# Performance work log

Hardware: AMD Instinct MI355X
Metric: run time of the kernel (lower is better)

Reference implementation:

```python
import jax, jax.numpy as jnp
import numpy as np

B, C, H, W = 4, 128, 128, 128
K = 9          # 3x3 kernel taps
TAU, BETA = 0.5, 10.0


def conv3x3(x, w, b):
    # x: (B,Cin,H,W), w: (Cout,Cin,3,3), stride 1, padding 1
    y = jax.lax.conv_general_dilated(
        x, w, window_strides=(1, 1), padding=((1, 1), (1, 1)),
        dimension_numbers=('NCHW', 'OIHW', 'NCHW'))
    return y + b[None, :, None, None]


def bilinear_sample(x, py, px):
    # x: (B,C,H,W); py,px: (B,K,H,W) fractional coords -> (B,C,K,H,W), zero outside
    Hi, Wi = x.shape[2], x.shape[3]
    y0 = jnp.floor(py); x0 = jnp.floor(px)
    y1 = y0 + 1.0;      x1 = x0 + 1.0
    ly = py - y0; lx = px - x0
    hy = 1.0 - ly; hx = 1.0 - lx
    xf = x.reshape(x.shape[0], x.shape[1], -1)  # (B,C,HW)

    def corner(yc, xc, wgt):
        valid = (yc >= 0) & (yc <= Hi - 1) & (xc >= 0) & (xc <= Wi - 1)
        yi = jnp.clip(yc, 0, Hi - 1).astype(jnp.int32)
        xi = jnp.clip(xc, 0, Wi - 1).astype(jnp.int32)
        idx = (yi * Wi + xi).reshape(yc.shape[0], -1)  # (B, K*H*W)
        g = jax.vmap(lambda f, i: f[:, i])(xf, idx)    # (B,C,K*H*W)
        g = g.reshape(x.shape[0], x.shape[1], *yc.shape[1:])  # (B,C,K,H,W)
        return g * (wgt * valid.astype(wgt.dtype))[:, None]

    return (corner(y0, x0, hy * hx) + corner(y0, x1, hy * lx)
            + corner(y1, x0, ly * hx) + corner(y1, x1, ly * lx))


def modulated_dcn(x, offset, mask, w, b):
    # offset: (B,2K,H,W) layout (dy,dx) per tap; mask: (B,K,H,W)
    Bn, Cn, Hn, Wn = x.shape
    off = offset.reshape(Bn, K, 2, Hn, Wn)
    dy, dx = off[:, :, 0], off[:, :, 1]
    ky, kx = jnp.meshgrid(jnp.arange(3), jnp.arange(3), indexing='ij')
    base_y = (ky.reshape(-1) - 1).astype(x.dtype)  # dilation=1, padding=1, stride=1
    base_x = (kx.reshape(-1) - 1).astype(x.dtype)
    hh = jnp.arange(Hn, dtype=x.dtype)
    ww = jnp.arange(Wn, dtype=x.dtype)
    py = hh[None, None, :, None] + base_y[None, :, None, None] + dy  # (B,K,H,W)
    px = ww[None, None, None, :] + base_x[None, :, None, None] + dx
    samp = bilinear_sample(x, py, px) * mask[:, None]  # (B,C,K,H,W)
    out = jnp.einsum('bckhw,ock->bohw', samp, w.reshape(w.shape[0], w.shape[1], K))
    return out + b[None, :, None, None]


def setup_inputs() -> dict:
    key = jax.random.key(0)
    ks = jax.random.split(key, 8)
    x = jax.random.normal(ks[0], (B, C, H, W), dtype=jnp.float32)
    U = jax.random.uniform(ks[1], (B, 1, H, W), dtype=jnp.float32)
    # conv_offset_mask: (3*K, C+1, 3, 3); small scale -> offsets of O(1) pixel
    w_om = jax.random.normal(ks[2], (3 * K, C + 1, 3, 3), dtype=jnp.float32) * 0.01
    b_om = jnp.zeros((3 * K,), dtype=jnp.float32)
    kaiming = float(np.sqrt(2.0 / (C * 9)))
    w_dcn = jax.random.normal(ks[3], (C, C, 3, 3), dtype=jnp.float32) * kaiming
    b_dcn = jnp.zeros((C,), dtype=jnp.float32)
    w1 = jax.random.normal(ks[4], (C, C, 3, 3), dtype=jnp.float32) * kaiming
    b1 = jnp.zeros((C,), dtype=jnp.float32)
    w2 = jax.random.normal(ks[5], (C, C, 3, 3), dtype=jnp.float32) * float(np.sqrt(1.0 / (C * 9)))
    b2 = jnp.zeros((C,), dtype=jnp.float32)
    return {"x": x, "U": U, "w_om": w_om, "b_om": b_om, "w_dcn": w_dcn,
            "b_dcn": b_dcn, "w1": w1, "b1": b1, "w2": w2, "b2": b2}


def reference(x, U, w_om, b_om, w_dcn, b_dcn, w1, b1, w2, b2):
    U = jnp.clip(U, 0.0, 1.0)
    guide = jnp.concatenate([x, U], axis=1)                # (B,C+1,H,W)
    om = conv3x3(guide, w_om, b_om)                        # (B,3K,H,W)
    offset = om[:, :2 * K]
    mask = 2.0 * jax.nn.sigmoid(om[:, 2 * K:])
    z = modulated_dcn(x, offset, mask, w_dcn, b_dcn)
    r = jax.nn.relu(conv3x3(z, w1, b1))
    r = conv3x3(r, w2, b2)
    gate = jax.nn.sigmoid(BETA * (U - TAU))
    return jax.nn.relu(x + r * gate)
```

## Files before the change

kernel.cpp:

```cpp
#include <hip/hip_runtime.h>
#include <math.h>

typedef unsigned int uint;
typedef unsigned short ushort;
typedef __attribute__((ext_vector_type(8))) __bf16 bf16x8;
typedef __attribute__((ext_vector_type(4))) float f32x4;

#define HW 16384

__device__ __forceinline__ ushort f2bf(float f) {
    uint u = __float_as_uint(f);
    u += 0x7fffu + ((u >> 16) & 1u);
    return (ushort)(u >> 16);
}
__device__ __forceinline__ void bhmap(int& b, int& h) {
    int lin = blockIdx.y * (int)gridDim.x + blockIdx.x;
    int n = (lin & 7) * 64 + (lin >> 3);
    h = n & 127;
    b = n >> 7;
}
__device__ __forceinline__ int swz(int row, int chunk) {
    return row * 128 + ((chunk ^ (row & 15)) << 3);
}
__device__ __forceinline__ uint blend2(uint a, uint b, uint c, uint d,
                                       float w00, float w01, float w10, float w11) {
    float lo = w00 * __uint_as_float(a << 16) + w01 * __uint_as_float(b << 16)
             + w10 * __uint_as_float(c << 16) + w11 * __uint_as_float(d << 16);
    float hi = w00 * __uint_as_float(a & 0xffff0000u) + w01 * __uint_as_float(b & 0xffff0000u)
             + w10 * __uint_as_float(c & 0xffff0000u) + w11 * __uint_as_float(d & 0xffff0000u);
    uint ul = __float_as_uint(lo); ul += 0x7fffu + ((ul >> 16) & 1u);
    uint uh = __float_as_uint(hi); uh += 0x7fffu + ((uh >> 16) & 1u);
    return (ul >> 16) | ((uh >> 16) << 16);
}

__global__ __launch_bounds__(256) void prep_w(
    const float* __restrict__ wd, const float* __restrict__ w1,
    const float* __restrict__ w2, const float* __restrict__ wom,
    ushort* __restrict__ wdt, ushort* __restrict__ w1t,
    ushort* __restrict__ w2t, ushort* __restrict__ womt,
    float* __restrict__ womu)
{
    int i = blockIdx.x * 256 + threadIdx.x;
    if (i < 147456) {
        int k = i >> 14, oc = (i >> 7) & 127, ci = i & 127;
        int s = (oc * 128 + ci) * 9 + k;
        wdt[i] = f2bf(wd[s]);
        w1t[i] = f2bf(w1[s]);
        w2t[i] = f2bf(w2[s]);
    }
    if (i < 36864) {
        int k = i >> 12, oc = (i >> 7) & 31, ci = i & 127;
        womt[i] = (oc < 27) ? f2bf(wom[(oc * 129 + ci) * 9 + k]) : (ushort)0;
    }
    if (i < 288) {
        int k = i >> 5, oc = i & 31;
        womu[i] = (oc < 27) ? wom[(oc * 129 + 128) * 9 + k] : 0.f;
    }
}

__global__ __launch_bounds__(256) void prep_xt(
    const float* __restrict__ x, ushort* __restrict__ xt)
{
    int b, h; bhmap(b, h);
    const int tid = threadIdx.x;
    __shared__ __align__(16) ushort T[128 * 136];
    const int w0 = tid & 127, cg = tid >> 7;
#pragma unroll 4
    for (int it = 0; it < 64; it++) {
        int c = it * 2 + cg;
        float f = x[((size_t)(b * 128 + c)) * HW + h * 128 + w0];
        T[w0 * 136 + c] = f2bf(f);
    }
    __syncthreads();
    const int w1 = tid >> 1, half = tid & 1;
    uint4* dst = (uint4*)(xt + (((size_t)b * HW) + h * 128 + w1) * 128 + half * 64);
    const uint4* src = (const uint4*)&T[w1 * 136 + half * 64];
#pragma unroll
    for (int c8 = 0; c8 < 8; c8++) dst[c8] = src[c8];
}

__global__ __launch_bounds__(512, 4) void k_om(
    const ushort* __restrict__ xt, const float* __restrict__ U,
    const ushort* __restrict__ womt, const float* __restrict__ womu,
    const float* __restrict__ bom, float* __restrict__ omt)
{
    int b, h; bhmap(b, h);
    const int tid = threadIdx.x;
    const int wid = tid >> 6, lane = tid & 63, lq = lane & 15, quad = lane >> 4;
    const int pixbase = wid * 16;

    __shared__ __align__(16) ushort As[128 * 128];
    __shared__ __align__(16) ushort Bs[32 * 128];
    __shared__ float U3[3 * 130];
    __shared__ float wu[288];

    f32x4 acc[2];
#pragma unroll
    for (int j = 0; j < 2; j++)
#pragma unroll
        for (int r = 0; r < 4; r++) acc[j][r] = 0.f;

    for (int s = tid; s < 390; s += 512) {
        int r = s / 130, c = s % 130, gy = h - 1 + r, gx = c - 1;
        float v = 0.f;
        if ((unsigned)gy < 128u && (unsigned)gx < 128u) {
            v = U[(size_t)b * HW + gy * 128 + gx];
            v = fminf(fmaxf(v, 0.f), 1.f);
        }
        U3[s] = v;
    }
    if (tid < 288) wu[tid] = womu[tid];

    const int arow = tid >> 2, aq = tid & 3;
    const int brow = tid >> 4, bchunk = tid & 15;
    for (int t9 = 0; t9 < 9; t9++) {
        int dy = t9 / 3 - 1, dx = t9 % 3 - 1;
        int gy = h + dy, gx = arow + dx;
        if ((unsigned)gy < 128u && (unsigned)gx < 128u) {
            const uint4* src = (const uint4*)(xt + (((size_t)b * HW) + gy * 128 + gx) * 128 + aq * 32);
#pragma unroll
            for (int c = 0; c < 4; c++) *(uint4*)&As[swz(arow, aq * 4 + c)] = src[c];
        } else {
            uint4 zz = {0, 0, 0, 0};
#pragma unroll
            for (int c = 0; c < 4; c++) *(uint4*)&As[swz(arow, aq * 4 + c)] = zz;
        }
        *(uint4*)&Bs[swz(brow, bchunk)] = *(const uint4*)(womt + t9 * 4096 + brow * 128 + bchunk * 8);
        __syncthreads();
#pragma unroll
        for (int kk = 0; kk < 4; kk++) {
            int chunk = kk * 4 + quad;
            bf16x8 av = *(const bf16x8*)&As[swz(pixbase + lq, chunk)];
            bf16x8 bv[2];
#pragma unroll
            for (int j = 0; j < 2; j++) bv[j] = *(const bf16x8*)&Bs[swz(j * 16 + lq, chunk)];
#pragma unroll
            for (int j = 0; j < 2; j++)
                acc[j] = __builtin_amdgcn_mfma_f32_16x16x32_bf16(av, bv[j], acc[j], 0, 0, 0);
        }
        __syncthreads();
    }

#pragma unroll
    for (int j = 0; j < 2; j++) {
        int oc = j * 16 + lq;
        if (oc < 27) {
            float bias = bom[oc];
#pragma unroll
            for (int r = 0; r < 4; r++) {
                int pix = pixbase + quad * 4 + r;
                float v = acc[j][r] + bias;
#pragma unroll
                for (int t = 0; t < 9; t++)
                    v += U3[(t / 3) * 130 + pix + (t % 3)] * wu[t * 32 + oc];
                if (oc >= 18) v = 2.f / (1.f + __expf(-v));
                omt[((size_t)b * HW + h * 128 + pix) * 32 + oc] = v;
            }
        }
    }
}

__global__ __launch_bounds__(512, 4) void k_dcn(
    const ushort* __restrict__ xt, const float* __restrict__ omt,
    const ushort* __restrict__ wdt, const float* __restrict__ bdcn,
    ushort* __restrict__ zt)
{
    int b, h; bhmap(b, h);
    const int tid = threadIdx.x;
    const int wid = tid >> 6, lane = tid & 63, lq = lane & 15, quad = lane >> 4;
    const int pixbase = (wid & 1) * 64, ocbase = (wid >> 1) * 32;

    __shared__ __align__(16) ushort As[128 * 128];
    __shared__ __align__(16) ushort Bs[128 * 128];
    __shared__ __align__(16) int tbl[2][128][8];

    const int sc = lane & 15;
    const int sp = lane >> 4;

    f32x4 acc[4][2];
#pragma unroll
    for (int i = 0; i < 4; i++)
#pragma unroll
        for (int j = 0; j < 2; j++)
#pragma unroll
            for (int r = 0; r < 4; r++) acc[i][j][r] = 0.f;

    const float* omrow = omt + ((size_t)b * HW + h * 128) * 32;
    const ushort* xtb = xt + (size_t)b * HW * 128;

    auto build = [&](int k, int buf) {
        if (tid < 128) {
            int p = tid;
            float dyv = omrow[p * 32 + 2 * k];
            float dxv = omrow[p * 32 + 2 * k + 1];
            float m   = omrow[p * 32 + 18 + k];
            float fy = (float)(h + k / 3 - 1) + dyv;
            float fx = (float)(p + k % 3 - 1) + dxv;
            float y0f = floorf(fy), x0f = floorf(fx);
            float ly = fy - y0f, lx = fx - x0f;
            float hy = 1.f - ly, hx = 1.f - lx;
            bool vy0 = (y0f >= 0.f) && (y0f <= 127.f);
            bool vy1 = (y0f >= -1.f) && (y0f <= 126.f);
            bool vx0 = (x0f >= 0.f) && (x0f <= 127.f);
            bool vx1 = (x0f >= -1.f) && (x0f <= 126.f);
            float w00 = (vy0 && vx0) ? hy * hx * m : 0.f;
            float w01 = (vy0 && vx1) ? hy * lx * m : 0.f;
            float w10 = (vy1 && vx0) ? ly * hx * m : 0.f;
            float w11 = (vy1 && vx1) ? ly * lx * m : 0.f;
            int iy0 = min(max((int)y0f, 0), 127);
            int iy1 = min(max((int)y0f + 1, 0), 127);
            int ix0 = min(max((int)x0f, 0), 127);
            int ix1 = min(max((int)x0f + 1, 0), 127);
            int* tp = &tbl[buf][p][0];
            tp[0] = (iy0 * 128 + ix0) * 128;
            tp[1] = (iy0 * 128 + ix1) * 128;
            tp[2] = (iy1 * 128 + ix0) * 128;
            tp[3] = (iy1 * 128 + ix1) * 128;
            ((float*)tp)[4] = w00; ((float*)tp)[5] = w01;
            ((float*)tp)[6] = w10; ((float*)tp)[7] = w11;
        }
    };

    build(0, 0);
    __syncthreads();

    const int brow = tid >> 2, bq = tid & 3;
    for (int k = 0; k < 9; k++) {
        const int buf = k & 1;
        {
            const uint4* src = (const uint4*)(wdt + (size_t)k * 16384 + brow * 128 + bq * 32);
#pragma unroll
            for (int c = 0; c < 4; c++) *(uint4*)&Bs[swz(brow, bq * 4 + c)] = src[c];
        }
        const ushort* basep = xtb + sc * 8;
#pragma unroll 2
        for (int r = 0; r < 4; r++) {
            int p = r * 32 + wid * 4 + sp;
            int4 off = *(const int4*)&tbl[buf][p][0];
            f32x4 wv = *(const f32x4*)((const float*)&tbl[buf][p][0] + 4);
            uint4 q00 = *(const uint4*)(basep + off.x);
            uint4 q01 = *(const uint4*)(basep + off.y);
            uint4 q10 = *(const uint4*)(basep + off.z);
            uint4 q11 = *(const uint4*)(basep + off.w);
            uint4 st;
            st.x = blend2(q00.x, q01.x, q10.x, q11.x, wv[0], wv[1], wv[2], wv[3]);
            st.y = blend2(q00.y, q01.y, q10.y, q11.y, wv[0], wv[1], wv[2], wv[3]);
            st.z = blend2(q00.z, q01.z, q10.z, q11.z, wv[0], wv[1], wv[2], wv[3]);
            st.w = blend2(q00.w, q01.w, q10.w, q11.w, wv[0], wv[1], wv[2], wv[3]);
            *(uint4*)&As[swz(p, sc)] = st;
        }
        __syncthreads();
        if (k < 8) build(k + 1, buf ^ 1);
#pragma unroll
        for (int kk = 0; kk < 4; kk++) {
            int chunk = kk * 4 + quad;
            bf16x8 av[4], bv[2];
#pragma unroll
            for (int i = 0; i < 4; i++) av[i] = *(const bf16x8*)&As[swz(pixbase + i * 16 + lq, chunk)];
#pragma unroll
            for (int j = 0; j < 2; j++) bv[j] = *(const bf16x8*)&Bs[swz(ocbase + j * 16 + lq, chunk)];
#pragma unroll
            for (int i = 0; i < 4; i++)
#pragma unroll
                for (int j = 0; j < 2; j++)
                    acc[i][j] = __builtin_amdgcn_mfma_f32_16x16x32_bf16(av[i], bv[j], acc[i][j], 0, 0, 0);
        }
        __syncthreads();
    }

    size_t prow = ((size_t)b * HW + h * 128) * 128;
#pragma unroll
    for (int j = 0; j < 2; j++) {
        int oc = ocbase + j * 16 + lq;
        float bias = bdcn[oc];
#pragma unroll
        for (int i = 0; i < 4; i++)
#pragma unroll
            for (int r = 0; r < 4; r++) {
                int pix = pixbase + i * 16 + quad * 4 + r;
                zt[prow + (size_t)pix * 128 + oc] = f2bf(acc[i][j][r] + bias);
            }
    }
}

__global__ __launch_bounds__(512, 4) void k_conv1(
    const ushort* __restrict__ zt, const ushort* __restrict__ w1t,
    const float* __restrict__ b1, ushort* __restrict__ r1t)
{
    int b, h; bhmap(b, h);
    const int tid = threadIdx.x;
    const int wid = tid >> 6, lane = tid & 63, lq = lane & 15, quad = lane >> 4;
    const int pixbase = (wid & 1) * 64, ocbase = (wid >> 1) * 32;

    __shared__ __align__(16) ushort As[128 * 128];
    __shared__ __align__(16) ushort Bs[128 * 128];

    f32x4 acc[4][2];
#pragma unroll
    for (int i = 0; i < 4; i++)
#pragma unroll
        for (int j = 0; j < 2; j++)
#pragma unroll
            for (int r = 0; r < 4; r++) acc[i][j][r] = 0.f;

    const int row = tid >> 2, q = tid & 3;
    for (int t9 = 0; t9 < 9; t9++) {
        int dy = t9 / 3 - 1, dx = t9 % 3 - 1;
        int gy = h + dy, gx = row + dx;
        if ((unsigned)gy < 128u && (unsigned)gx < 128u) {
            const uint4* src = (const uint4*)(zt + (((size_t)b * HW) + gy * 128 + gx) * 128 + q * 32);
#pragma unroll
            for (int c = 0; c < 4; c++) *(uint4*)&As[swz(row, q * 4 + c)] = src[c];
        } else {
            uint4 zz = {0, 0, 0, 0};
#pragma unroll
            for (int c = 0; c < 4; c++) *(uint4*)&As[swz(row, q * 4 + c)] = zz;
        }
        {
            const uint4* src = (const uint4*)(w1t + (size_t)t9 * 16384 + row * 128 + q * 32);
#pragma unroll
            for (int c = 0; c < 4; c++) *(uint4*)&Bs[swz(row, q * 4 + c)] = src[c];
        }
        __syncthreads();
#pragma unroll
        for (int kk = 0; kk < 4; kk++) {
            int chunk = kk * 4 + quad;
            bf16x8 av[4], bv[2];
#pragma unroll
            for (int i = 0; i < 4; i++) av[i] = *(const bf16x8*)&As[swz(pixbase + i * 16 + lq, chunk)];
#pragma unroll
            for (int j = 0; j < 2; j++) bv[j] = *(const bf16x8*)&Bs[swz(ocbase + j * 16 + lq, chunk)];
#pragma unroll
            for (int i = 0; i < 4; i++)
#pragma unroll
                for (int j = 0; j < 2; j++)
                    acc[i][j] = __builtin_amdgcn_mfma_f32_16x16x32_bf16(av[i], bv[j], acc[i][j], 0, 0, 0);
        }
        __syncthreads();
    }

    size_t prow = ((size_t)b * HW + h * 128) * 128;
#pragma unroll
    for (int j = 0; j < 2; j++) {
        int oc = ocbase + j * 16 + lq;
        float bias = b1[oc];
#pragma unroll
        for (int i = 0; i < 4; i++)
#pragma unroll
            for (int r = 0; r < 4; r++) {
                int pix = pixbase + i * 16 + quad * 4 + r;
                r1t[prow + (size_t)pix * 128 + oc] = f2bf(fmaxf(acc[i][j][r] + bias, 0.f));
            }
    }
}

__global__ __launch_bounds__(512, 4) void k_conv2(
    const ushort* __restrict__ r1t, const ushort* __restrict__ w2t,
    const float* __restrict__ b2, const float* __restrict__ x,
    const float* __restrict__ U, float* __restrict__ out)
{
    int b, h; bhmap(b, h);
    const int tid = threadIdx.x;
    const int wid = tid >> 6, lane = tid & 63, lq = lane & 15, quad = lane >> 4;
    const int mbase = (wid & 1) * 64;
    const int nbase = (wid >> 1) * 32;

    __shared__ __align__(16) ushort As[128 * 128];
    __shared__ __align__(16) ushort Bs[128 * 128];

    f32x4 acc[4][2];
#pragma unroll
    for (int i = 0; i < 4; i++)
#pragma unroll
        for (int j = 0; j < 2; j++)
#pragma unroll
            for (int r = 0; r < 4; r++) acc[i][j][r] = 0.f;

    const int row = tid >> 2, q = tid & 3;
    for (int t9 = 0; t9 < 9; t9++) {
        int dy = t9 / 3 - 1, dx = t9 % 3 - 1;
        {
            const uint4* src = (const uint4*)(w2t + (size_t)t9 * 16384 + row * 128 + q * 32);
#pragma unroll
            for (int c = 0; c < 4; c++) *(uint4*)&As[swz(row, q * 4 + c)] = src[c];
        }
        int gy = h + dy, gx = row + dx;
        if ((unsigned)gy < 128u && (unsigned)gx < 128u) {
            const uint4* src = (const uint4*)(r1t + (((size_t)b * HW) + gy * 128 + gx) * 128 + q * 32);
#pragma unroll
            for (int c = 0; c < 4; c++) *(uint4*)&Bs[swz(row, q * 4 + c)] = src[c];
        } else {
            uint4 zz = {0, 0, 0, 0};
#pragma unroll
            for (int c = 0; c < 4; c++) *(uint4*)&Bs[swz(row, q * 4 + c)] = zz;
        }
        __syncthreads();
#pragma unroll
        for (int kk = 0; kk < 4; kk++) {
            int chunk = kk * 4 + quad;
            bf16x8 av[4], bv[2];
#pragma unroll
            for (int i = 0; i < 4; i++) av[i] = *(const bf16x8*)&As[swz(mbase + i * 16 + lq, chunk)];
#pragma unroll
            for (int j = 0; j < 2; j++) bv[j] = *(const bf16x8*)&Bs[swz(nbase + j * 16 + lq, chunk)];
#pragma unroll
            for (int i = 0; i < 4; i++)
#pragma unroll
                for (int j = 0; j < 2; j++)
                    acc[i][j] = __builtin_amdgcn_mfma_f32_16x16x32_bf16(av[i], bv[j], acc[i][j], 0, 0, 0);
        }
        __syncthreads();
    }

#pragma unroll
    for (int j = 0; j < 2; j++) {
        int pix = nbase + j * 16 + lq;
        float u = U[(size_t)b * HW + h * 128 + pix];
        u = fminf(fmaxf(u, 0.f), 1.f);
        float g = 1.f / (1.f + __expf(-10.f * (u - 0.5f)));
#pragma unroll
        for (int i = 0; i < 4; i++) {
            f32x4 b4 = *(const f32x4*)&b2[mbase + i * 16 + quad * 4];
#pragma unroll
            for (int r = 0; r < 4; r++) {
                int oc = mbase + i * 16 + quad * 4 + r;
                size_t idx = ((size_t)(b * 128 + oc)) * HW + h * 128 + pix;
                float v = acc[i][j][r] + b4[r];
                out[idx] = fmaxf(x[idx] + v * g, 0.f);
            }
        }
    }
}

extern "C" void kernel_launch(void* const* d_in, const int* in_sizes, int n_in,
                              void* d_out, int out_size, void* d_ws, size_t ws_size,
                              hipStream_t stream)
{
    const float* x     = (const float*)d_in[0];
    const float* U     = (const float*)d_in[1];
    const float* w_om  = (const float*)d_in[2];
    const float* b_om  = (const float*)d_in[3];
    const float* w_dcn = (const float*)d_in[4];
    const float* b_dcn = (const float*)d_in[5];
    const float* w1    = (const float*)d_in[6];
    const float* b1    = (const float*)d_in[7];
    const float* w2    = (const float*)d_in[8];
    const float* b2    = (const float*)d_in[9];
    float* out = (float*)d_out;

    char* p = (char*)d_ws;
    ushort* xt   = (ushort*)p; p += (size_t)4 * HW * 128 * 2;
    ushort* zt   = (ushort*)p; p += (size_t)4 * HW * 128 * 2;
    ushort* r1t  = (ushort*)p; p += (size_t)4 * HW * 128 * 2;
    float*  omt  = (float*)p;  p += (size_t)4 * HW * 32 * 4;
    ushort* wdt  = (ushort*)p; p += 147456 * 2;
    ushort* w1t  = (ushort*)p; p += 147456 * 2;
    ushort* w2t  = (ushort*)p; p += 147456 * 2;
    ushort* womt = (ushort*)p; p += 36864 * 2;
    float*  womu = (float*)p;  p += 288 * 4;

    prep_w<<<576, 256, 0, stream>>>(w_dcn, w1, w2, w_om, wdt, w1t, w2t, womt, womu);
    prep_xt<<<dim3(128, 4), 256, 0, stream>>>(x, xt);
    k_om<<<dim3(128, 4), 512, 0, stream>>>(xt, U, womt, womu, b_om, omt);
    k_dcn<<<dim3(128, 4), 512, 0, stream>>>(xt, omt, wdt, b_dcn, zt);
    k_conv1<<<dim3(128, 4), 512, 0, stream>>>(zt, w1t, b1, r1t);
    k_conv2<<<dim3(128, 4), 512, 0, stream>>>(r1t, w2t, b2, x, U, out);
}
```

Baseline: 233.5 us.

## Stage 3x66-pixel halo once per block and read conv weights directly from global

The three 3x3 convolution kernels (om, conv1, conv2) now use 256-thread blocks over half-row tiles of 64 pixels. Each block stages a 3x66 halo of the input once into LDS, so the input is no longer reloaded per tap and the per-tap barriers go away. Weights in the om, conv1, conv2 and DCN kernels are read straight from global memory (through cache) into MFMA operands instead of being copied to LDS. This cuts LDS use and syncs, and k_dcn's occupancy hint is raised from 4 to 6. The cost is uncoalesced global weight loads sitting in the MFMA inner loop, plus halo redundancy from the smaller tiles.

```diff
diff --git a/kernel.cpp b/kernel.cpp
--- a/kernel.cpp
+++ b/kernel.cpp
@@ -18,6 +18,14 @@
     int n = (lin & 7) * 64 + (lin >> 3);
     h = n & 127;
     b = n >> 7;
+}
+__device__ __forceinline__ void bhmap2(int& b, int& h, int& px0) {
+    int lin = blockIdx.x;
+    int n = ((lin & 7) << 7) | (lin >> 3);
+    b = n >> 8;
+    int rm = n & 255;
+    h = rm >> 1;
+    px0 = (rm & 1) << 6;
 }
 __device__ __forceinline__ int swz(int row, int chunk) {
     return row * 128 + ((chunk ^ (row & 15)) << 3);
@@ -79,29 +87,42 @@
     for (int c8 = 0; c8 < 8; c8++) dst[c8] = src[c8];
 }
 
-__global__ __launch_bounds__(512, 4) void k_om(
+__device__ __forceinline__ void stage_halo(
+    ushort* Hs, const ushort* __restrict__ src, int b, int h, int px0, int tid, int nthr)
+{
+    for (int s = tid; s < 396; s += nthr) {
+        int r = s >> 1, half = s & 1;
+        int ky = r / 66, xi = r - ky * 66;
+        int gy = h - 1 + ky, gx = px0 - 1 + xi;
+        if ((unsigned)gy < 128u && (unsigned)gx < 128u) {
+            const uint4* p = (const uint4*)(src + (((size_t)b * HW) + gy * 128 + gx) * 128 + half * 64);
+#pragma unroll
+            for (int c = 0; c < 8; c++) *(uint4*)&Hs[swz(r, half * 8 + c)] = p[c];
+        } else {
+            uint4 zz = {0, 0, 0, 0};
+#pragma unroll
+            for (int c = 0; c < 8; c++) *(uint4*)&Hs[swz(r, half * 8 + c)] = zz;
+        }
+    }
+}
+
+__global__ __launch_bounds__(256, 3) void k_om(
     const ushort* __restrict__ xt, const float* __restrict__ U,
     const ushort* __restrict__ womt, const float* __restrict__ womu,
     const float* __restrict__ bom, float* __restrict__ omt)
 {
-    int b, h; bhmap(b, h);
+    int b, h, px0; bhmap2(b, h, px0);
     const int tid = threadIdx.x;
     const int wid = tid >> 6, lane = tid & 63, lq = lane & 15, quad = lane >> 4;
-    const int pixbase = wid * 16;
-
-    __shared__ __align__(16) ushort As[128 * 128];
-    __shared__ __align__(16) ushort Bs[32 * 128];
-    __shared__ float U3[3 * 130];
+
+    __shared__ __align__(16) ushort Hs[198 * 128];
+    __shared__ float U3[3 * 66];
     __shared__ float wu[288];
 
-    f32x4 acc[2];
-#pragma unroll
-    for (int j = 0; j < 2; j++)
-#pragma unroll
-        for (int r = 0; r < 4; r++) acc[j][r] = 0.f;
-
-    for (int s = tid; s < 390; s += 512) {
-        int r = s / 130, c = s % 130, gy = h - 1 + r, gx = c - 1;
+    stage_halo(Hs, xt, b, h, px0, tid, 256);
+    for (int s = tid; s < 198; s += 256) {
+        int ky = s / 66, xi = s - ky * 66;
+        int gy = h - 1 + ky, gx = px0 - 1 + xi;
         float v = 0.f;
         if ((unsigned)gy < 128u && (unsigned)gx < 128u) {
             v = U[(size_t)b * HW + gy * 128 + gx];
@@ -109,37 +130,34 @@
         }
         U3[s] = v;
     }
-    if (tid < 288) wu[tid] = womu[tid];
-
-    const int arow = tid >> 2, aq = tid & 3;
-    const int brow = tid >> 4, bchunk = tid & 15;
-    for (int t9 = 0; t9 < 9; t9++) {
-        int dy = t9 / 3 - 1, dx = t9 % 3 - 1;
-        int gy = h + dy, gx = arow + dx;
-        if ((unsigned)gy < 128u && (unsigned)gx < 128u) {
-            const uint4* src = (const uint4*)(xt + (((size_t)b * HW) + gy * 128 + gx) * 128 + aq * 32);
-#pragma unroll
-            for (int c = 0; c < 4; c++) *(uint4*)&As[swz(arow, aq * 4 + c)] = src[c];
-        } else {
-            uint4 zz = {0, 0, 0, 0};
-#pragma unroll
-            for (int c = 0; c < 4; c++) *(uint4*)&As[swz(arow, aq * 4 + c)] = zz;
-        }
-        *(uint4*)&Bs[swz(brow, bchunk)] = *(const uint4*)(womt + t9 * 4096 + brow * 128 + bchunk * 8);
-        __syncthreads();
-#pragma unroll
-        for (int kk = 0; kk < 4; kk++) {
-            int chunk = kk * 4 + quad;
-            bf16x8 av = *(const bf16x8*)&As[swz(pixbase + lq, chunk)];
-            bf16x8 bv[2];
-#pragma unroll
-            for (int j = 0; j < 2; j++) bv[j] = *(const bf16x8*)&Bs[swz(j * 16 + lq, chunk)];
-#pragma unroll
-            for (int j = 0; j < 2; j++)
-                acc[j] = __builtin_amdgcn_mfma_f32_16x16x32_bf16(av, bv[j], acc[j], 0, 0, 0);
-        }
-        __syncthreads();
-    }
+    for (int s = tid; s < 288; s += 256) wu[s] = womu[s];
+    __syncthreads();
+
+    f32x4 acc[2];
+#pragma unroll
+    for (int j = 0; j < 2; j++)
+#pragma unroll
+        for (int r = 0; r < 4; r++) acc[j][r] = 0.f;
+
+#pragma unroll
+    for (int ky = 0; ky < 3; ky++)
+#pragma unroll
+        for (int kx = 0; kx < 3; kx++) {
+            const ushort* wt = womt + (ky * 3 + kx) * 4096;
+            const int base = ky * 66 + kx + wid * 16;
+#pragma unroll
+            for (int kk = 0; kk < 4; kk++) {
+                int chunk = kk * 4 + quad;
+                bf16x8 bv[2];
+#pragma unroll
+                for (int j = 0; j < 2; j++)
+                    bv[j] = *(const bf16x8*)(wt + (j * 16 + lq) * 128 + chunk * 8);
+                bf16x8 av = *(const bf16x8*)&Hs[swz(base + lq, chunk)];
+#pragma unroll
+                for (int j = 0; j < 2; j++)
+                    acc[j] = __builtin_amdgcn_mfma_f32_16x16x32_bf16(av, bv[j], acc[j], 0, 0, 0);
+            }
+        }
 
 #pragma unroll
     for (int j = 0; j < 2; j++) {
@@ -148,19 +166,19 @@
             float bias = bom[oc];
 #pragma unroll
             for (int r = 0; r < 4; r++) {
-                int pix = pixbase + quad * 4 + r;
+                int pix = wid * 16 + quad * 4 + r;
                 float v = acc[j][r] + bias;
 #pragma unroll
                 for (int t = 0; t < 9; t++)
-                    v += U3[(t / 3) * 130 + pix + (t % 3)] * wu[t * 32 + oc];
+                    v += U3[(t / 3) * 66 + pix + (t % 3)] * wu[t * 32 + oc];
                 if (oc >= 18) v = 2.f / (1.f + __expf(-v));
-                omt[((size_t)b * HW + h * 128 + pix) * 32 + oc] = v;
-            }
-        }
-    }
-}
-
-__global__ __launch_bounds__(512, 4) void k_dcn(
+                omt[((size_t)b * HW + h * 128 + px0 + pix) * 32 + oc] = v;
+            }
+        }
+    }
+}
+
+__global__ __launch_bounds__(512, 6) void k_dcn(
     const ushort* __restrict__ xt, const float* __restrict__ omt,
     const ushort* __restrict__ wdt, const float* __restrict__ bdcn,
     ushort* __restrict__ zt)
@@ -171,7 +189,6 @@
     const int pixbase = (wid & 1) * 64, ocbase = (wid >> 1) * 32;
 
     __shared__ __align__(16) ushort As[128 * 128];
-    __shared__ __align__(16) ushort Bs[128 * 128];
     __shared__ __align__(16) int tbl[2][128][8];
 
     const int sc = lane & 15;
@@ -224,14 +241,8 @@
     build(0, 0);
     __syncthreads();
 
-    const int brow = tid >> 2, bq = tid & 3;
     for (int k = 0; k < 9; k++) {
         const int buf = k & 1;
-        {
-            const uint4* src = (const uint4*)(wdt + (size_t)k * 16384 + brow * 128 + bq * 32);
-#pragma unroll
-            for (int c = 0; c < 4; c++) *(uint4*)&Bs[swz(brow, bq * 4 + c)] = src[c];
-        }
         const ushort* basep = xtb + sc * 8;
 #pragma unroll 2
         for (int r = 0; r < 4; r++) {
@@ -251,14 +262,16 @@
         }
         __syncthreads();
         if (k < 8) build(k + 1, buf ^ 1);
+        const ushort* wt = wdt + (size_t)k * 16384;
 #pragma unroll
         for (int kk = 0; kk < 4; kk++) {
             int chunk = kk * 4 + quad;
             bf16x8 av[4], bv[2];
 #pragma unroll
+            for (int j = 0; j < 2; j++)
+                bv[j] = *(const bf16x8*)(wt + (ocbase + j * 16 + lq) * 128 + chunk * 8);
+#pragma unroll
             for (int i = 0; i < 4; i++) av[i] = *(const bf16x8*)&As[swz(pixbase + i * 16 + lq, chunk)];
-#pragma unroll
-            for (int j = 0; j < 2; j++) bv[j] = *(const bf16x8*)&Bs[swz(ocbase + j * 16 + lq, chunk)];
 #pragma unroll
             for (int i = 0; i < 4; i++)
 #pragma unroll
@@ -283,17 +296,19 @@
     }
 }
 
-__global__ __launch_bounds__(512, 4) void k_conv1(
+__global__ __launch_bounds__(256, 3) void k_conv1(
     const ushort* __restrict__ zt, const ushort* __restrict__ w1t,
     const float* __restrict__ b1, ushort* __restrict__ r1t)
 {
-    int b, h; bhmap(b, h);
+    int b, h, px0; bhmap2(b, h, px0);
     const int tid = threadIdx.x;
     const int wid = tid >> 6, lane = tid & 63, lq = lane & 15, quad = lane >> 4;
-    const int pixbase = (wid & 1) * 64, ocbase = (wid >> 1) * 32;
-
-    __shared__ __align__(16) ushort As[128 * 128];
-    __shared__ __align__(16) ushort Bs[128 * 128];
+    const int ocbase = wid * 32;
+
+    __shared__ __align__(16) ushort Hs[198 * 128];
+
+    stage_halo(Hs, zt, b, h, px0, tid, 256);
+    __syncthreads();
 
     f32x4 acc[4][2];
 #pragma unroll
@@ -303,43 +318,32 @@
 #pragma unroll
             for (int r = 0; r < 4; r++) acc[i][j][r] = 0.f;
 
-    const int row = tid >> 2, q = tid & 3;
-    for (int t9 = 0; t9 < 9; t9++) {
-        int dy = t9 / 3 - 1, dx = t9 % 3 - 1;
-        int gy = h + dy, gx = row + dx;
-        if ((unsigned)gy < 128u && (unsigned)gx < 128u) {
-            const uint4* src = (const uint4*)(zt + (((size_t)b * HW) + gy * 128 + gx) * 128 + q * 32);
-#pragma unroll
-            for (int c = 0; c < 4; c++) *(uint4*)&As[swz(row, q * 4 + c)] = src[c];
-        } else {
-            uint4 zz = {0, 0, 0, 0};
-#pragma unroll
-            for (int c = 0; c < 4; c++) *(uint4*)&As[swz(row, q * 4 + c)] = zz;
-        }
-        {
-            const uint4* src = (const uint4*)(w1t + (size_t)t9 * 16384 + row * 128 + q * 32);
-#pragma unroll
-            for (int c = 0; c < 4; c++) *(uint4*)&Bs[swz(row, q * 4 + c)] = src[c];
-        }
-        __syncthreads();
-#pragma unroll
-        for (int kk = 0; kk < 4; kk++) {
-            int chunk = kk * 4 + quad;
-            bf16x8 av[4], bv[2];
-#pragma unroll
-            for (int i = 0; i < 4; i++) av[i] = *(const bf16x8*)&As[swz(pixbase + i * 16 + lq, chunk)];
-#pragma unroll
-            for (int j = 0; j < 2; j++) bv[j] = *(const bf16x8*)&Bs[swz(ocbase + j * 16 + lq, chunk)];
-#pragma unroll
-            for (int i = 0; i < 4; i++)
+#pragma unroll
+    for (int ky = 0; ky < 3; ky++)
+#pragma unroll
+        for (int kx = 0; kx < 3; kx++) {
+            const ushort* wt = w1t + (size_t)(ky * 3 + kx) * 16384;
+            const int base = ky * 66 + kx;
+#pragma unroll
+            for (int kk = 0; kk < 4; kk++) {
+                int chunk = kk * 4 + quad;
+                bf16x8 bv[2];
 #pragma unroll
                 for (int j = 0; j < 2; j++)
-                    acc[i][j] = __builtin_amdgcn_mfma_f32_16x16x32_bf16(av[i], bv[j], acc[i][j], 0, 0, 0);
-        }
-        __syncthreads();
-    }
-
-    size_t prow = ((size_t)b * HW + h * 128) * 128;
+                    bv[j] = *(const bf16x8*)(wt + (ocbase + j * 16 + lq) * 128 + chunk * 8);
+                bf16x8 av[4];
+#pragma unroll
+                for (int i = 0; i < 4; i++)
+                    av[i] = *(const bf16x8*)&Hs[swz(base + i * 16 + lq, chunk)];
+#pragma unroll
+                for (int i = 0; i < 4; i++)
+#pragma unroll
+                    for (int j = 0; j < 2; j++)
+                        acc[i][j] = __builtin_amdgcn_mfma_f32_16x16x32_bf16(av[i], bv[j], acc[i][j], 0, 0, 0);
+            }
+        }
+
+    size_t prow = ((size_t)b * HW + h * 128 + px0) * 128;
 #pragma unroll
     for (int j = 0; j < 2; j++) {
         int oc = ocbase + j * 16 + lq;
@@ -348,83 +352,72 @@
         for (int i = 0; i < 4; i++)
 #pragma unroll
             for (int r = 0; r < 4; r++) {
-                int pix = pixbase + i * 16 + quad * 4 + r;
+                int pix = i * 16 + quad * 4 + r;
                 r1t[prow + (size_t)pix * 128 + oc] = f2bf(fmaxf(acc[i][j][r] + bias, 0.f));
             }
     }
 }
 
-__global__ __launch_bounds__(512, 4) void k_conv2(
+__global__ __launch_bounds__(256, 3) void k_conv2(
     const ushort* __restrict__ r1t, const ushort* __restrict__ w2t,
     const float* __restrict__ b2, const float* __restrict__ x,
     const float* __restrict__ U, float* __restrict__ out)
 {
-    int b, h; bhmap(b, h);
+    int b, h, px0; bhmap2(b, h, px0);
     const int tid = threadIdx.x;
     const int wid = tid >> 6, lane = tid & 63, lq = lane & 15, quad = lane >> 4;
-    const int mbase = (wid & 1) * 64;
-    const int nbase = (wid >> 1) * 32;
-
-    __shared__ __align__(16) ushort As[128 * 128];
-    __shared__ __align__(16) ushort Bs[128 * 128];
-
-    f32x4 acc[4][2];
-#pragma unroll
-    for (int i = 0; i < 4; i++)
-#pragma unroll
-        for (int j = 0; j < 2; j++)
+    const int ocbase = wid * 32;
+
+    __shared__ __align__(16) ushort Hs[198 * 128];
+
+    stage_halo(Hs, r1t, b, h, px0, tid, 256);
+    __syncthreads();
+
+    f32x4 acc[2][4];
+#pragma unroll
+    for (int i = 0; i < 2; i++)
+#pragma unroll
+        for (int j = 0; j < 4; j++)
 #pragma unroll
             for (int r = 0; r < 4; r++) acc[i][j][r] = 0.f;
 
-    const int row = tid >> 2, q = tid & 3;
-    for (int t9 = 0; t9 < 9; t9++) {
-        int dy = t9 / 3 - 1, dx = t9 % 3 - 1;
-        {
-            const uint4* src = (const uint4*)(w2t + (size_t)t9 * 16384 + row * 128 + q * 32);
-#pragma unroll
-            for (int c = 0; c < 4; c++) *(uint4*)&As[swz(row, q * 4 + c)] = src[c];
-        }
-        int gy = h + dy, gx = row + dx;
-        if ((unsigned)gy < 128u && (unsigned)gx < 128u) {
-            const uint4* src = (const uint4*)(r1t + (((size_t)b * HW) + gy * 128 + gx) * 128 + q * 32);
-#pragma unroll
-            for (int c = 0; c < 4; c++) *(uint4*)&Bs[swz(row, q * 4 + c)] = src[c];
-        } else {
-            uint4 zz = {0, 0, 0, 0};
-#pragma unroll
-            for (int c = 0; c < 4; c++) *(uint4*)&Bs[swz(row, q * 4 + c)] = zz;
-        }
-        __syncthreads();
-#pragma unroll
-        for (int kk = 0; kk < 4; kk++) {
-            int chunk = kk * 4 + quad;
-            bf16x8 av[4], bv[2];
-#pragma unroll
-            for (int i = 0; i < 4; i++) av[i] = *(const bf16x8*)&As[swz(mbase + i * 16 + lq, chunk)];
-#pragma unroll
-            for (int j = 0; j < 2; j++) bv[j] = *(const bf16x8*)&Bs[swz(nbase + j * 16 + lq, chunk)];
-#pragma unroll
-            for (int i = 0; i < 4; i++)
-#pragma unroll
-                for (int j = 0; j < 2; j++)
-                    acc[i][j] = __builtin_amdgcn_mfma_f32_16x16x32_bf16(av[i], bv[j], acc[i][j], 0, 0, 0);
-        }
-        __syncthreads();
-    }
-
-#pragma unroll
-    for (int j = 0; j < 2; j++) {
-        int pix = nbase + j * 16 + lq;
-        float u = U[(size_t)b * HW + h * 128 + pix];
+#pragma unroll
+    for (int ky = 0; ky < 3; ky++)
+#pragma unroll
+        for (int kx = 0; kx < 3; kx++) {
+            const ushort* wt = w2t + (size_t)(ky * 3 + kx) * 16384;
+            const int base = ky * 66 + kx;
+#pragma unroll
+            for (int kk = 0; kk < 4; kk++) {
+                int chunk = kk * 4 + quad;
+                bf16x8 av[2], bv[4];
+#pragma unroll
+                for (int i = 0; i < 2; i++)
+                    av[i] = *(const bf16x8*)(wt + (ocbase + i * 16 + lq) * 128 + chunk * 8);
+#pragma unroll
+                for (int j = 0; j < 4; j++)
+                    bv[j] = *(const bf16x8*)&Hs[swz(base + j * 16 + lq, chunk)];
+#pragma unroll
+                for (int i = 0; i < 2; i++)
+#pragma unroll
+                    for (int j = 0; j < 4; j++)
+                        acc[i][j] = __builtin_amdgcn_mfma_f32_16x16x32_bf16(av[i], bv[j], acc[i][j], 0, 0, 0);
+            }
+        }
+
+#pragma unroll
+    for (int j = 0; j < 4; j++) {
+        int pix = j * 16 + lq;
+        float u = U[(size_t)b * HW + h * 128 + px0 + pix];
         u = fminf(fmaxf(u, 0.f), 1.f);
         float g = 1.f / (1.f + __expf(-10.f * (u - 0.5f)));
 #pragma unroll
-        for (int i = 0; i < 4; i++) {
-            f32x4 b4 = *(const f32x4*)&b2[mbase + i * 16 + quad * 4];
+        for (int i = 0; i < 2; i++) {
+            f32x4 b4 = *(const f32x4*)&b2[ocbase + i * 16 + quad * 4];
 #pragma unroll
             for (int r = 0; r < 4; r++) {
-                int oc = mbase + i * 16 + quad * 4 + r;
-                size_t idx = ((size_t)(b * 128 + oc)) * HW + h * 128 + pix;
+                int oc = ocbase + i * 16 + quad * 4 + r;
+                size_t idx = ((size_t)(b * 128 + oc)) * HW + h * 128 + px0 + pix;
                 float v = acc[i][j][r] + b4[r];
                 out[idx] = fmaxf(x[idx] + v * g, 0.f);
             }
@@ -461,8 +454,8 @@
 
     prep_w<<<576, 256, 0, stream>>>(w_dcn, w1, w2, w_om, wdt, w1t, w2t, womt, womu);
     prep_xt<<<dim3(128, 4), 256, 0, stream>>>(x, xt);
-    k_om<<<dim3(128, 4), 512, 0, stream>>>(xt, U, womt, womu, b_om, omt);
+    k_om<<<1024, 256, 0, stream>>>(xt, U, womt, womu, b_om, omt);
     k_dcn<<<dim3(128, 4), 512, 0, stream>>>(xt, omt, wdt, b_dcn, zt);
-    k_conv1<<<dim3(128, 4), 512, 0, stream>>>(zt, w1t, b1, r1t);
-    k_conv2<<<dim3(128, 4), 512, 0, stream>>>(r1t, w2t, b2, x, U, out);
-}
+    k_conv1<<<1024, 256, 0, stream>>>(zt, w1t, b1, r1t);
+    k_conv2<<<1024, 256, 0, stream>>>(r1t, w2t, b2, x, U, out);
+}
```

Result: slower. 347.3 us (+48.8%).
